# Kernel tuning notes

Measured on AMD Instinct MI355X. Metric: run time of the kernel, lower is better.

The kernel has to match this reference:

```python
import jax, jax.numpy as jnp
import numpy as np

N_NODES = 50000


def setup_inputs() -> dict:
    key = jax.random.key(0)
    k1, k2, k3, k4, k5, k6 = jax.random.split(key, 6)
    features = jax.random.normal(k1, (N_NODES, 128), dtype=jnp.float32)
    anchor_distances = jax.random.uniform(k2, (N_NODES, 64), dtype=jnp.float32)
    W = jax.random.normal(k3, (192, 128), dtype=jnp.float32) * (1.0 / np.sqrt(192.0))
    b = jax.random.normal(k4, (128,), dtype=jnp.float32) * 0.01
    src = jax.random.randint(k5, (800000,), 0, N_NODES, dtype=jnp.int32)
    dst = jax.random.randint(k6, (800000,), 0, N_NODES, dtype=jnp.int32)
    return {"features": features, "anchor_distances": anchor_distances,
            "W": W, "b": b, "src": src, "dst": dst}


def reference(features, anchor_distances, W, b, src, dst):
    # Linear(in_feats + num_anchors -> hidden) + ReLU
    combined = jnp.concatenate([features, anchor_distances], axis=1)  # [N, 192]
    h = jax.nn.relu(combined @ W + b)                                  # [N, H]
    # copy_u + mean aggregation: mean of h[src] grouped by dst
    msg_sum = jax.ops.segment_sum(h[src], dst, num_segments=N_NODES)  # [N, H]
    deg = jax.ops.segment_sum(jnp.ones_like(dst, dtype=h.dtype), dst,
                              num_segments=N_NODES)                    # [N]
    # DGL mean leaves 0 for isolated nodes; divide by max(deg, 1)
    out = msg_sum / jnp.maximum(deg, 1.0)[:, None]
    return out
```

## Files before the change

### kernel.cpp

```cpp
#include <hip/hip_runtime.h>
#include <hip/hip_bf16.h>


#define N_NODES 50000
#define N_EDGES 800000
#define HID 128
#define FDIM 128
#define ADIM 64
#define KDIM 192

#define BKT_SH 5
#define BKT_NODES 32
#define NBUCKETS ((N_NODES + BKT_NODES - 1) / BKT_NODES)
#define CAP 1024
#define PC_NBLK 256
#define PC_CHUNK ((N_EDGES + PC_NBLK - 1) / PC_NBLK)
#define EPT 13
#define GEMM_NBLK ((N_NODES + 31) / 32)
#define SA_LD 200

typedef __attribute__((ext_vector_type(8))) short short8;
typedef __attribute__((ext_vector_type(4))) float f32x4;
typedef __attribute__((ext_vector_type(4))) unsigned int u32x4;

__device__ inline unsigned short f2bf(float f) {
  unsigned u = __float_as_uint(f);
  u += 0x7FFFu + ((u >> 16) & 1u);
  return (unsigned short)(u >> 16);
}
__device__ inline unsigned pk2bf(float a, float b) {
  return (unsigned)f2bf(a) | ((unsigned)f2bf(b) << 16);
}
__device__ inline float bf2f(unsigned short s) {
  return __uint_as_float(((unsigned)s) << 16);
}

__global__ __launch_bounds__(256) void wbt_kernel(
    const float* __restrict__ W, unsigned short* __restrict__ WbTf,
    int* __restrict__ bcur) {
  if (blockIdx.x == 0) {
    for (int i = threadIdx.x; i < NBUCKETS; i += 256) bcur[i] = 0;
  }
  int idx = blockIdx.x * 256 + threadIdx.x;
  if (idx >= 2 * 4 * 6 * 64 * 8) return;
  int j = idx & 7;
  int lane = (idx >> 3) & 63;
  int frag = idx >> 9;
  int kk = frag % 6, p = frag / 6;
  int wn = p >> 2, nt = p & 3;
  int col = wn * 64 + nt * 16 + (lane & 15);
  int k = kk * 32 + (lane >> 4) * 8 + j;
  WbTf[idx] = f2bf(W[k * HID + col]);
}

#define SMEM_BYTES (32 * SA_LD * 2)
__global__ __launch_bounds__(256) void gemm_pscatter_kernel(
    const float* __restrict__ F, const float* __restrict__ A,
    const unsigned short* __restrict__ WbTf, const float* __restrict__ bias,
    unsigned short* __restrict__ hb,
    const int* __restrict__ src, const int* __restrict__ dst,
    int* __restrict__ bcur, unsigned* __restrict__ edata, int nrows) {
  __shared__ __align__(16) char smem_raw[SMEM_BYTES];

  if (blockIdx.x < PC_NBLK) {
    int* lh = (int*)smem_raw;
    int* lc = lh + NBUCKETS;
    int bp = blockIdx.x;
    for (int i = threadIdx.x; i < NBUCKETS; i += 256) lh[i] = 0;
    __syncthreads();
    int base = bp * PC_CHUNK;
    int end = base + PC_CHUNK; if (end > N_EDGES) end = N_EDGES;
    int rd[EPT], rs[EPT];
#pragma unroll
    for (int k = 0; k < EPT; ++k) {
      int j = base + threadIdx.x + k * 256;
      if (j < end) {
        rd[k] = dst[j];
        rs[k] = src[j];
        atomicAdd(&lh[rd[k] >> BKT_SH], 1);
      } else {
        rd[k] = -1;
      }
    }
    __syncthreads();
    for (int i = threadIdx.x; i < NBUCKETS; i += 256) {
      int c = lh[i];
      lh[i] = c ? atomicAdd(&bcur[i], c) : 0;
      lc[i] = 0;
    }
    __syncthreads();
#pragma unroll
    for (int k = 0; k < EPT; ++k) {
      if (rd[k] >= 0) {
        int bk = rd[k] >> BKT_SH, dl = rd[k] & (BKT_NODES - 1);
        int p = lh[bk] + atomicAdd(&lc[bk], 1);
        if (p < CAP)
          edata[(bk << 10) + p] = (unsigned)rs[k] | ((unsigned)dl << 16);
      }
    }
    return;
  }

  unsigned short* sA = (unsigned short*)smem_raw;
  const int gblk = blockIdx.x - PC_NBLK;
  const int tid = threadIdx.x;
  const int lane = tid & 63;
  const int wave = tid >> 6;
  const int wm = wave >> 1, wn = wave & 1;
  const int l15 = lane & 15, lg = lane >> 4;
  const int blockrow = gblk * 32;

#pragma unroll
  for (int it = 0; it < 4; ++it) {
    int i = tid + it * 256;
    int row = i >> 5, c4 = (i & 31) * 4;
    int crow = blockrow + row; crow = crow < nrows ? crow : (nrows - 1);
    float4 v = *(const float4*)(F + (size_t)crow * FDIM + c4);
    *(uint2*)(sA + row * SA_LD + c4) = make_uint2(pk2bf(v.x, v.y), pk2bf(v.z, v.w));
  }
#pragma unroll
  for (int it = 0; it < 2; ++it) {
    int i = tid + it * 256;
    int row = i >> 4, c4 = (i & 15) * 4;
    int crow = blockrow + row; crow = crow < nrows ? crow : (nrows - 1);
    float4 v = *(const float4*)(A + (size_t)crow * ADIM + c4);
    *(uint2*)(sA + row * SA_LD + FDIM + c4) = make_uint2(pk2bf(v.x, v.y), pk2bf(v.z, v.w));
  }

  short8 Bf[24];
#pragma unroll
  for (int nt = 0; nt < 4; ++nt)
#pragma unroll
    for (int kk = 0; kk < 6; ++kk)
      Bf[nt * 6 + kk] = *(const short8*)(
          WbTf + ((((wn * 4 + nt) * 6 + kk) << 9) + (lane << 3)));

  __syncthreads();

  short8 Af[6];
  const int rowl = wm * 16 + l15;
#pragma unroll
  for (int kk = 0; kk < 6; ++kk)
    Af[kk] = *(const short8*)(sA + rowl * SA_LD + kk * 32 + lg * 8);

  f32x4 acc[4] = {{0,0,0,0},{0,0,0,0},{0,0,0,0},{0,0,0,0}};
#pragma unroll
  for (int nt = 0; nt < 4; ++nt)
#pragma unroll
    for (int kk = 0; kk < 6; ++kk)
      acc[nt] = __builtin_amdgcn_mfma_f32_16x16x32_bf16(
          Af[kk], Bf[nt * 6 + kk], acc[nt], 0, 0, 0);

  const int rowbase = blockrow + wm * 16;
#pragma unroll
  for (int nt = 0; nt < 4; ++nt) {
    int col = wn * 64 + nt * 16 + l15;
    float bv = bias[col];
#pragma unroll
    for (int q = 0; q < 4; ++q) {
      int row = rowbase + lg * 4 + q;
      if (row < nrows) {
        float v = fmaxf(acc[nt][q] + bv, 0.f);
        hb[(size_t)row * HID + col] = f2bf(v);
      }
    }
  }
}

__device__ inline int wave_incl_scan(int v, int lane) {
#pragma unroll
  for (int off = 1; off < 64; off <<= 1) {
    int t = __shfl_up(v, off, 64);
    if (lane >= off) v += t;
  }
  return v;
}

#define EPT_A (CAP / 256)
__global__ __launch_bounds__(256) void bucket_agg_kernel(
    const unsigned short* __restrict__ hb, const int* __restrict__ bcur,
    const unsigned* __restrict__ edata, float* __restrict__ out) {
  int b = blockIdx.x;
  int nbase = b << BKT_SH;
  int nloc = N_NODES - nbase; if (nloc > BKT_NODES) nloc = BKT_NODES;
  int gb = b << 10;
  int cnt = bcur[b]; cnt = cnt < CAP ? cnt : CAP;
  int t = threadIdx.x, lane = t & 63, wave = t >> 6;
  int g = lane >> 4, l16 = lane & 15;

  __shared__ unsigned short ss[CAP];
  __shared__ int loff[BKT_NODES + 1];
  __shared__ int lcnt[BKT_NODES];
  __shared__ int lcur[BKT_NODES];

  unsigned er[EPT_A];
  if (t < BKT_NODES) lcnt[t] = 0;
  __syncthreads();
#pragma unroll
  for (int k = 0; k < EPT_A; ++k) {
    int j = t + k * 256;
    if (j < cnt) {
      er[k] = edata[gb + j];
      atomicAdd(&lcnt[er[k] >> 16], 1);
    } else {
      er[k] = 0xFFFFFFFFu;
    }
  }
  __syncthreads();
  if (wave == 0) {
    int v = (lane < BKT_NODES) ? lcnt[lane] : 0;
    int incl = wave_incl_scan(v, lane);
    if (lane < BKT_NODES) {
      loff[lane + 1] = incl;
      lcur[lane] = incl - v;
    }
    if (lane == 0) loff[0] = 0;
  }
  __syncthreads();
#pragma unroll
  for (int k = 0; k < EPT_A; ++k) {
    if (er[k] != 0xFFFFFFFFu) {
      int p = atomicAdd(&lcur[er[k] >> 16], 1);
      ss[p] = (unsigned short)(er[k] & 0xFFFFu);
    }
  }
  __syncthreads();
  for (int n = wave; n < nloc; n += 4) {
    int s0 = loff[n], s1 = loff[n + 1];
    float acc[8] = {0, 0, 0, 0, 0, 0, 0, 0};
    int j = s0 + g;
    for (; j + 4 < s1; j += 8) {
      int e0 = ss[j], e1 = ss[j + 4];
      u32x4 v0 = *(const u32x4*)(hb + (size_t)e0 * HID + l16 * 8);
      u32x4 v1 = *(const u32x4*)(hb + (size_t)e1 * HID + l16 * 8);
#pragma unroll
      for (int i = 0; i < 4; ++i) {
        unsigned w0 = v0[i], w1 = v1[i];
        acc[2 * i]     += bf2f((unsigned short)(w0 & 0xFFFFu))
                        + bf2f((unsigned short)(w1 & 0xFFFFu));
        acc[2 * i + 1] += bf2f((unsigned short)(w0 >> 16))
                        + bf2f((unsigned short)(w1 >> 16));
      }
    }
    if (j < s1) {
      int e0 = ss[j];
      u32x4 v0 = *(const u32x4*)(hb + (size_t)e0 * HID + l16 * 8);
#pragma unroll
      for (int i = 0; i < 4; ++i) {
        unsigned w0 = v0[i];
        acc[2 * i]     += bf2f((unsigned short)(w0 & 0xFFFFu));
        acc[2 * i + 1] += bf2f((unsigned short)(w0 >> 16));
      }
    }
#pragma unroll
    for (int i = 0; i < 8; ++i) {
      acc[i] += __shfl_xor(acc[i], 16, 64);
      acc[i] += __shfl_xor(acc[i], 32, 64);
    }
    if (g == 0) {
      int d = s1 - s0;
      float inv = 1.0f / (float)(d > 1 ? d : 1);
      float* po = out + (size_t)(nbase + n) * HID + l16 * 8;
      *(float4*)po       = make_float4(acc[0]*inv, acc[1]*inv, acc[2]*inv, acc[3]*inv);
      *(float4*)(po + 4) = make_float4(acc[4]*inv, acc[5]*inv, acc[6]*inv, acc[7]*inv);
    }
  }
}

extern "C" void kernel_launch(void* const* d_in, const int* in_sizes, int n_in,
                              void* d_out, int out_size, void* d_ws, size_t ws_size,
                              hipStream_t stream) {
  const float* F   = (const float*)d_in[0];
  const float* A   = (const float*)d_in[1];
  const float* W   = (const float*)d_in[2];
  const float* b   = (const float*)d_in[3];
  const int*   src = (const int*)d_in[4];
  const int*   dst = (const int*)d_in[5];
  float* out = (float*)d_out;

  char* ws = (char*)d_ws;
  size_t off = 0;
  auto alloc = [&](size_t bytes) {
    char* p = ws + off;
    off += (bytes + 255) & ~(size_t)255;
    return p;
  };
  unsigned short* hb   = (unsigned short*)alloc((size_t)N_NODES * HID * 2);
  unsigned short* WbTf = (unsigned short*)alloc((size_t)HID * KDIM * 2);
  int* bcur = (int*)alloc((size_t)NBUCKETS * sizeof(int));
  unsigned* edata = (unsigned*)alloc((size_t)NBUCKETS * CAP * sizeof(unsigned));
  (void)ws_size;

  wbt_kernel<<<(KDIM * HID + 255) / 256, 256, 0, stream>>>(W, WbTf, bcur);
  gemm_pscatter_kernel<<<PC_NBLK + GEMM_NBLK, 256, 0, stream>>>(
      F, A, WbTf, b, hb, src, dst, bcur, edata, N_NODES);
  bucket_agg_kernel<<<NBUCKETS, 256, 0, stream>>>(hb, bcur, edata, out);
}
```

Measured before the change: 67.05 us.

## Load GEMM A fragments directly from global, add nontemporal hints, unroll gather by 4

```diff
diff --git a/kernel.cpp b/kernel.cpp
--- a/kernel.cpp
+++ b/kernel.cpp
@@ -17,7 +17,6 @@
 #define PC_CHUNK ((N_EDGES + PC_NBLK - 1) / PC_NBLK)
 #define EPT 13
 #define GEMM_NBLK ((N_NODES + 31) / 32)
-#define SA_LD 200
 
 typedef __attribute__((ext_vector_type(8))) short short8;
 typedef __attribute__((ext_vector_type(4))) float f32x4;
@@ -33,6 +32,12 @@
 }
 __device__ inline float bf2f(unsigned short s) {
   return __uint_as_float(((unsigned)s) << 16);
+}
+__device__ inline short8 pack8(f32x4 a, f32x4 b) {
+  union { short8 s; u32x4 u; } cv;
+  cv.u = (u32x4){pk2bf(a[0], a[1]), pk2bf(a[2], a[3]),
+                 pk2bf(b[0], b[1]), pk2bf(b[2], b[3])};
+  return cv.s;
 }
 
 __global__ __launch_bounds__(256) void wbt_kernel(
@@ -53,7 +58,7 @@
   WbTf[idx] = f2bf(W[k * HID + col]);
 }
 
-#define SMEM_BYTES (32 * SA_LD * 2)
+#define SMEM_BYTES (((2 * NBUCKETS * 4) + 255) & ~255)
 __global__ __launch_bounds__(256) void gemm_pscatter_kernel(
     const float* __restrict__ F, const float* __restrict__ A,
     const unsigned short* __restrict__ WbTf, const float* __restrict__ bias,
@@ -75,8 +80,8 @@
     for (int k = 0; k < EPT; ++k) {
       int j = base + threadIdx.x + k * 256;
       if (j < end) {
-        rd[k] = dst[j];
-        rs[k] = src[j];
+        rd[k] = __builtin_nontemporal_load(dst + j);
+        rs[k] = __builtin_nontemporal_load(src + j);
         atomicAdd(&lh[rd[k] >> BKT_SH], 1);
       } else {
         rd[k] = -1;
@@ -101,7 +106,6 @@
     return;
   }
 
-  unsigned short* sA = (unsigned short*)smem_raw;
   const int gblk = blockIdx.x - PC_NBLK;
   const int tid = threadIdx.x;
   const int lane = tid & 63;
@@ -110,23 +114,6 @@
   const int l15 = lane & 15, lg = lane >> 4;
   const int blockrow = gblk * 32;
 
-#pragma unroll
-  for (int it = 0; it < 4; ++it) {
-    int i = tid + it * 256;
-    int row = i >> 5, c4 = (i & 31) * 4;
-    int crow = blockrow + row; crow = crow < nrows ? crow : (nrows - 1);
-    float4 v = *(const float4*)(F + (size_t)crow * FDIM + c4);
-    *(uint2*)(sA + row * SA_LD + c4) = make_uint2(pk2bf(v.x, v.y), pk2bf(v.z, v.w));
-  }
-#pragma unroll
-  for (int it = 0; it < 2; ++it) {
-    int i = tid + it * 256;
-    int row = i >> 4, c4 = (i & 15) * 4;
-    int crow = blockrow + row; crow = crow < nrows ? crow : (nrows - 1);
-    float4 v = *(const float4*)(A + (size_t)crow * ADIM + c4);
-    *(uint2*)(sA + row * SA_LD + FDIM + c4) = make_uint2(pk2bf(v.x, v.y), pk2bf(v.z, v.w));
-  }
-
   short8 Bf[24];
 #pragma unroll
   for (int nt = 0; nt < 4; ++nt)
@@ -135,13 +122,23 @@
       Bf[nt * 6 + kk] = *(const short8*)(
           WbTf + ((((wn * 4 + nt) * 6 + kk) << 9) + (lane << 3)));
 
-  __syncthreads();
-
+  int r = blockrow + wm * 16 + l15;
+  if (r >= nrows) r = nrows - 1;
+  const float* Frow = F + (size_t)r * FDIM + lg * 8;
+  const float* Arow = A + (size_t)r * ADIM + lg * 8;
   short8 Af[6];
-  const int rowl = wm * 16 + l15;
-#pragma unroll
-  for (int kk = 0; kk < 6; ++kk)
-    Af[kk] = *(const short8*)(sA + rowl * SA_LD + kk * 32 + lg * 8);
+#pragma unroll
+  for (int kk = 0; kk < 4; ++kk) {
+    f32x4 v0 = __builtin_nontemporal_load((const f32x4*)(Frow + kk * 32));
+    f32x4 v1 = __builtin_nontemporal_load((const f32x4*)(Frow + kk * 32 + 4));
+    Af[kk] = pack8(v0, v1);
+  }
+#pragma unroll
+  for (int kk = 0; kk < 2; ++kk) {
+    f32x4 v0 = __builtin_nontemporal_load((const f32x4*)(Arow + kk * 32));
+    f32x4 v1 = __builtin_nontemporal_load((const f32x4*)(Arow + kk * 32 + 4));
+    Af[4 + kk] = pack8(v0, v1);
+  }
 
   f32x4 acc[4] = {{0,0,0,0},{0,0,0,0},{0,0,0,0},{0,0,0,0}};
 #pragma unroll
@@ -200,7 +197,7 @@
   for (int k = 0; k < EPT_A; ++k) {
     int j = t + k * 256;
     if (j < cnt) {
-      er[k] = edata[gb + j];
+      er[k] = __builtin_nontemporal_load(edata + gb + j);
       atomicAdd(&lcnt[er[k] >> 16], 1);
     } else {
       er[k] = 0xFFFFFFFFu;
@@ -225,26 +222,33 @@
     }
   }
   __syncthreads();
+  const unsigned short* hbl = hb + l16 * 8;
   for (int n = wave; n < nloc; n += 4) {
     int s0 = loff[n], s1 = loff[n + 1];
     float acc[8] = {0, 0, 0, 0, 0, 0, 0, 0};
     int j = s0 + g;
-    for (; j + 4 < s1; j += 8) {
-      int e0 = ss[j], e1 = ss[j + 4];
-      u32x4 v0 = *(const u32x4*)(hb + (size_t)e0 * HID + l16 * 8);
-      u32x4 v1 = *(const u32x4*)(hb + (size_t)e1 * HID + l16 * 8);
+    for (; j + 12 < s1; j += 16) {
+      int e0 = ss[j], e1 = ss[j + 4], e2 = ss[j + 8], e3 = ss[j + 12];
+      u32x4 v0 = *(const u32x4*)(hbl + (size_t)e0 * HID);
+      u32x4 v1 = *(const u32x4*)(hbl + (size_t)e1 * HID);
+      u32x4 v2 = *(const u32x4*)(hbl + (size_t)e2 * HID);
+      u32x4 v3 = *(const u32x4*)(hbl + (size_t)e3 * HID);
 #pragma unroll
       for (int i = 0; i < 4; ++i) {
-        unsigned w0 = v0[i], w1 = v1[i];
-        acc[2 * i]     += bf2f((unsigned short)(w0 & 0xFFFFu))
-                        + bf2f((unsigned short)(w1 & 0xFFFFu));
-        acc[2 * i + 1] += bf2f((unsigned short)(w0 >> 16))
-                        + bf2f((unsigned short)(w1 >> 16));
-      }
-    }
-    if (j < s1) {
+        unsigned w0 = v0[i], w1 = v1[i], w2 = v2[i], w3 = v3[i];
+        acc[2 * i]     += (bf2f((unsigned short)(w0 & 0xFFFFu))
+                         + bf2f((unsigned short)(w1 & 0xFFFFu)))
+                        + (bf2f((unsigned short)(w2 & 0xFFFFu))
+                         + bf2f((unsigned short)(w3 & 0xFFFFu)));
+        acc[2 * i + 1] += (bf2f((unsigned short)(w0 >> 16))
+                         + bf2f((unsigned short)(w1 >> 16)))
+                        + (bf2f((unsigned short)(w2 >> 16))
+                         + bf2f((unsigned short)(w3 >> 16)));
+      }
+    }
+    for (; j < s1; j += 4) {
       int e0 = ss[j];
-      u32x4 v0 = *(const u32x4*)(hb + (size_t)e0 * HID + l16 * 8);
+      u32x4 v0 = *(const u32x4*)(hbl + (size_t)e0 * HID);
 #pragma unroll
       for (int i = 0; i < 4; ++i) {
         unsigned w0 = v0[i];
@@ -261,8 +265,10 @@
       int d = s1 - s0;
       float inv = 1.0f / (float)(d > 1 ? d : 1);
       float* po = out + (size_t)(nbase + n) * HID + l16 * 8;
-      *(float4*)po       = make_float4(acc[0]*inv, acc[1]*inv, acc[2]*inv, acc[3]*inv);
-      *(float4*)(po + 4) = make_float4(acc[4]*inv, acc[5]*inv, acc[6]*inv, acc[7]*inv);
+      f32x4 o0 = {acc[0] * inv, acc[1] * inv, acc[2] * inv, acc[3] * inv};
+      f32x4 o1 = {acc[4] * inv, acc[5] * inv, acc[6] * inv, acc[7] * inv};
+      __builtin_nontemporal_store(o0, (f32x4*)po);
+      __builtin_nontemporal_store(o1, (f32x4*)(po + 4));
     }
   }
 }
```

New measurement: 76.01 us. 1.13x slower.
